# Kernel optimization log

Hardware: AMD Instinct MI355X
Metric: run time of the kernel (lower is better)

The kernel has to match this reference:

```python
import jax, jax.numpy as jnp
import numpy as np

B, S, D, H, DFF = 4, 2048, 512, 8, 2048
HD = D // H  # head dim = 64
LN_EPS = 1e-5


def setup_inputs() -> dict:
    key = jax.random.key(0)
    ks = jax.random.split(key, 12)
    sc = 0.02
    return {
        "x": jax.random.normal(ks[0], (B, S, D), jnp.float32),
        "Wq": jax.random.normal(ks[1], (D, D), jnp.float32) * sc,
        "bq": jnp.zeros((D,), jnp.float32),
        "Wk": jax.random.normal(ks[2], (D, D), jnp.float32) * sc,
        "bk": jnp.zeros((D,), jnp.float32),
        "Wv": jax.random.normal(ks[3], (D, D), jnp.float32) * sc,
        "bv": jnp.zeros((D,), jnp.float32),
        "W1": jax.random.normal(ks[4], (D, DFF), jnp.float32) * sc,
        "b1": jnp.zeros((DFF,), jnp.float32),
        "W2": jax.random.normal(ks[5], (DFF, D), jnp.float32) * sc,
        "b2": jnp.zeros((D,), jnp.float32),
        "gamma": jnp.ones((D,), jnp.float32),
        "beta": jnp.zeros((D,), jnp.float32),
    }


def reference(x, Wq, bq, Wk, bk, Wv, bv, W1, b1, W2, b2, gamma, beta):
    # Multi-head self-attention (explicit bmm -> softmax -> bmm chain)
    q = (x @ Wq + bq).reshape(B, S, H, HD)
    k = (x @ Wk + bk).reshape(B, S, H, HD)
    v = (x @ Wv + bv).reshape(B, S, H, HD)
    scores = jnp.einsum("bqhd,bkhd->bhqk", q, k) / jnp.sqrt(jnp.float32(HD))
    atn = jax.nn.softmax(scores, axis=-1)          # [B,H,S,S]
    attn_out = jnp.einsum("bhqk,bkhd->bqhd", atn, v).reshape(B, S, D)
    # FFN with residual + LayerNorm (residual around FFN only, as in source)
    h = jax.nn.relu(attn_out @ W1 + b1)
    y = h @ W2 + b2 + attn_out
    mu = jnp.mean(y, axis=-1, keepdims=True)
    var = jnp.var(y, axis=-1, keepdims=True)
    out = (y - mu) * jax.lax.rsqrt(var + LN_EPS) * gamma + beta
    return (out, atn)
```

## Files before the change

kernel.cpp:

```cpp
#include <hip/hip_runtime.h>
#include <hip/hip_bf16.h>

#define TPB 256
typedef long long ll;


using short8  = __attribute__((ext_vector_type(8))) short;
using floatx4 = __attribute__((ext_vector_type(4))) float;

__device__ __forceinline__ unsigned short f2bu(float f) {
    union { float f; unsigned int u; } v; v.f = f;
    unsigned int u = v.u;
    return (unsigned short)((u + 0x7fffu + ((u >> 16) & 1u)) >> 16);
}

__device__ __forceinline__ float bu2f(unsigned short us) {
    union { unsigned int u; float f; } v; v.u = ((unsigned int)us) << 16;
    return v.f;
}

__device__ __forceinline__ unsigned int cvtpk(float lo, float hi) {
    unsigned int r;
    asm volatile("v_cvt_pk_bf16_f32 %0, %1, %2" : "=v"(r) : "v"(lo), "v"(hi));
    return r;
}

__device__ __forceinline__ void gload16(const unsigned short* g, unsigned short* l) {
    __builtin_amdgcn_global_load_lds(
        (const __attribute__((address_space(1))) void*)g,
        (__attribute__((address_space(3))) void*)l, 16, 0, 0);
}

template<int BM, int BN, int EPI>
__device__ __forceinline__ void gemm_body(
    const unsigned short* __restrict__ Ap, const unsigned short* __restrict__ BTp,
    const float* __restrict__ bias, void* __restrict__ Cp,
    const unsigned short* __restrict__ Rb,
    int K, ll lda, ll ldb, ll ldc, int bx, int by,
    unsigned short* Asm, unsigned short* Bsm)
{
    constexpr int BK = 64;
    const int tid  = threadIdx.x;
    const int lane = tid & 63;
    const int wave = tid >> 6;
    const int wm = wave >> 1, wn = wave & 1;
    constexpr int WM = BM / 2, WN = BN / 2, FM = WM / 16, FN = WN / 16;

    const ll brow = (ll)bx * BM;
    const ll bcol = (ll)by * BN;
    const int srow = lane >> 3, scol = (lane & 7) << 3;

    floatx4 acc[FM][FN] = {};

    for (int k0 = 0; k0 < K; k0 += BK) {
        #pragma unroll
        for (int ii = 0; ii < BM / 32; ++ii) {
            int i = wave + ii * 4;
            gload16(Ap + (brow + i * 8 + srow) * lda + k0 + scol, Asm + i * 512);
        }
        #pragma unroll
        for (int ii = 0; ii < BN / 32; ++ii) {
            int i = wave + ii * 4;
            gload16(BTp + (bcol + i * 8 + srow) * ldb + k0 + scol, Bsm + i * 512);
        }
        __syncthreads();

        #pragma unroll
        for (int kk = 0; kk < BK; kk += 32) {
            short8 af[FM], bfr[FN];
            const int kidx = kk + ((lane >> 4) << 3);
            const int ar = wm * WM + (lane & 15);
            const int bc = wn * WN + (lane & 15);
            #pragma unroll
            for (int m = 0; m < FM; m++)
                af[m] = *(const short8*)&Asm[(ar + m * 16) * BK + kidx];
            #pragma unroll
            for (int n = 0; n < FN; n++)
                bfr[n] = *(const short8*)&Bsm[(bc + n * 16) * BK + kidx];
            #pragma unroll
            for (int m = 0; m < FM; m++)
                #pragma unroll
                for (int n = 0; n < FN; n++)
                    acc[m][n] = __builtin_amdgcn_mfma_f32_16x16x32_bf16(af[m], bfr[n], acc[m][n], 0, 0, 0);
        }
        __syncthreads();
    }

    const ll crow0 = brow + wm * WM + ((lane >> 4) << 2);
    const ll ccol0 = bcol + wn * WN + (lane & 15);
    #pragma unroll
    for (int m = 0; m < FM; m++) {
        #pragma unroll
        for (int j = 0; j < 4; j++) {
            ll row = crow0 + m * 16 + j;
            #pragma unroll
            for (int np = 0; np < FN; np += 2) {
                ll col0 = ccol0 + np * 16;
                ll col1 = col0 + 16;
                float v0 = acc[m][np][j]     + bias[col0];
                float v1 = acc[m][np + 1][j] + bias[col1];
                if constexpr (EPI == 3) {
                    v0 = v0 > 0.f ? v0 : 0.f;
                    v1 = v1 > 0.f ? v1 : 0.f;
                } else if constexpr (EPI == 6) {
                    v0 += bu2f(Rb[row * ldc + col0]);
                    v1 += bu2f(Rb[row * ldc + col1]);
                }
                unsigned int r = cvtpk(v0, v1);
                ((unsigned short*)Cp)[row * ldc + col0] = (unsigned short)r;
                ((unsigned short*)Cp)[row * ldc + col1] = (unsigned short)(r >> 16);
            }
        }
    }
}

template<int BM, int BN, int EPI>
__global__ __launch_bounds__(TPB) void gemm_k(
    const unsigned short* __restrict__ Ap, const unsigned short* __restrict__ BTp,
    const float* __restrict__ bias, void* __restrict__ Cp,
    const unsigned short* __restrict__ Rb,
    int K, ll lda, ll ldb, ll ldc)
{
    __shared__ unsigned short sh[BM * 64 + BN * 64];
    int nwg = gridDim.x * gridDim.y;
    int sid = blockIdx.y * gridDim.x + blockIdx.x;
    int cpx = nwg >> 3;
    int w = (sid & 7) * cpx + (sid >> 3);
    int bx = w % gridDim.x, by = w / gridDim.x;
    gemm_body<BM, BN, EPI>(Ap, BTp, bias, Cp, Rb, K, lda, ldb, ldc, bx, by,
                           sh, sh + BM * 64);
}

__device__ __forceinline__ void atnwrite_body(
    const unsigned short* __restrict__ qkv, const float* __restrict__ ilbuf,
    float* __restrict__ atn, int BH0, int n, unsigned short* sh)
{
    unsigned short* Qsm = sh;
    unsigned short* Ksm = sh + 8192;
    float* Pst = (float*)sh;

    const int tid = threadIdx.x, lane = tid & 63, wave = tid >> 6;
    const int c0 = lane & 15, g = lane >> 4;
    const int bh = BH0 + (n & 7) * 2 + ((n >> 3) & 1);
    const int qt = n >> 4;
    const int b = bh >> 3, h = bh & 7;

    const ll qbase  = ((ll)(b * 2048 + qt * 128)) * 1536 + h * 64;
    const ll kbase0 = ((ll)(b * 2048)) * 1536 + 512 + h * 64;
    const int srow = lane >> 3, scol = (lane & 7) << 3;

    #pragma unroll
    for (int ii = 0; ii < 4; ++ii) {
        int i = wave + ii * 4;
        gload16(qkv + qbase + (ll)(i * 8 + srow) * 1536 + scol, Qsm + i * 512);
    }
    __syncthreads();
    short8 qf[2][2];
    #pragma unroll
    for (int nq = 0; nq < 2; nq++)
        #pragma unroll
        for (int kk = 0; kk < 2; kk++)
            qf[nq][kk] = *(const short8*)&Qsm[(wave * 32 + nq * 16 + c0) * 64 + kk * 32 + g * 8];

    float il2[2];
    #pragma unroll
    for (int nq = 0; nq < 2; nq++)
        il2[nq] = ilbuf[(ll)bh * 2048 + qt * 128 + wave * 32 + nq * 16 + c0];

    float* myP = Pst + wave * 1024;

    for (int kb = 0; kb < 16; ++kb) {
        const ll koff = kbase0 + (ll)kb * 128 * 1536;
        #pragma unroll
        for (int ii = 0; ii < 4; ++ii) {
            int i = wave + ii * 4;
            gload16(qkv + koff + (ll)(i * 8 + srow) * 1536 + scol, Ksm + i * 512);
        }
        __syncthreads();

        floatx4 sacc[8][2] = {};
        #pragma unroll
        for (int kk = 0; kk < 2; kk++)
            #pragma unroll
            for (int mk = 0; mk < 8; mk++) {
                short8 kf = *(const short8*)&Ksm[(mk * 16 + c0) * 64 + kk * 32 + g * 8];
                #pragma unroll
                for (int nq = 0; nq < 2; nq++)
                    sacc[mk][nq] = __builtin_amdgcn_mfma_f32_16x16x32_bf16(kf, qf[nq][kk], sacc[mk][nq], 0, 0, 0);
            }

        #pragma unroll
        for (int mk = 0; mk < 8; mk++)
            #pragma unroll
            for (int nq = 0; nq < 2; nq++)
                #pragma unroll
                for (int r = 0; r < 4; r++)
                    sacc[mk][nq][r] = __expf(sacc[mk][nq][r] * 0.125f) * il2[nq];

        #pragma unroll
        for (int nq = 0; nq < 2; nq++) {
            #pragma unroll
            for (int hf = 0; hf < 2; hf++) {
                if ((c0 >> 3) == hf) {
                    int rho = c0 & 7;
                    #pragma unroll
                    for (int mk = 0; mk < 8; mk++) {
                        int k4 = mk * 4 + g;
                        ((floatx4*)myP)[rho * 32 + (k4 ^ rho)] = sacc[mk][nq];
                    }
                }
                const ll grow = (ll)bh * 2048 + qt * 128 + wave * 32 + nq * 16 + hf * 8;
                #pragma unroll
                for (int t = 0; t < 4; t++) {
                    int rr = t * 2 + (lane >> 5);
                    int k4r = lane & 31;
                    floatx4 v = ((const floatx4*)myP)[rr * 32 + (k4r ^ rr)];
                    __builtin_nontemporal_store(
                        v, (floatx4*)(atn + (grow + rr) * 2048 + kb * 128 + k4r * 4));
                }
            }
        }
        __syncthreads();
    }
}

__global__ __launch_bounds__(TPB) void attn1_k(
    const unsigned short* __restrict__ qkv, const unsigned short* __restrict__ vt,
    unsigned short* __restrict__ attnb, float* __restrict__ ilbuf)
{
    __shared__ unsigned short sh[32768];

    const int tid = threadIdx.x, lane = tid & 63, wave = tid >> 6;
    const int c0 = lane & 15, g = lane >> 4;
    const int srow = lane >> 3, scol = (lane & 7) << 3;

    const int raw = blockIdx.x + blockIdx.y * 16;
    const int n   = raw >> 3;
    const int bh  = (raw & 7) * 4 + (n >> 4);
    const int qt  = n & 15;
    const int b = bh >> 3, h = bh & 7;

    const ll qbase  = ((ll)(b * 2048 + qt * 128)) * 1536 + h * 64;
    const ll kbase0 = ((ll)(b * 2048)) * 1536 + 512 + h * 64;
    const unsigned short* vbase = vt + (ll)bh * 64 * 2048;

    #pragma unroll
    for (int ii = 0; ii < 4; ++ii) {
        int i = wave + ii * 4;
        gload16(qkv + qbase + (ll)(i * 8 + srow) * 1536 + scol, sh + i * 512);
    }
    __syncthreads();
    short8 qf[2][2];
    #pragma unroll
    for (int nq = 0; nq < 2; nq++)
        #pragma unroll
        for (int kk = 0; kk < 2; kk++)
            qf[nq][kk] = *(const short8*)&sh[(wave * 32 + nq * 16 + c0) * 64 + kk * 32 + g * 8];
    __syncthreads();

    floatx4 oaccT[4][2] = {};
    float l_run[2] = {0.f, 0.f};

    const int srcA = c0 + ((g & 1) << 5);
    const int srcB = srcA + 16;
    const bool hiG = (g >= 2);

#define STAGE_KV(kbx, bb) do {                                                   \
    const ll koff_ = kbase0 + (ll)(kbx) * 128 * 1536;                            \
    unsigned short* Kd_ = sh + ((bb) << 13);                                     \
    unsigned short* Vd_ = sh + 16384 + ((bb) << 13);                             \
    _Pragma("unroll")                                                            \
    for (int ii = 0; ii < 4; ++ii) { int i = wave + ii * 4;                      \
        gload16(qkv + koff_ + (ll)(i * 8 + srow) * 1536 + scol, Kd_ + i * 512); }\
    _Pragma("unroll")                                                            \
    for (int ii = 0; ii < 4; ++ii) { int i = wave + ii * 4; int s = i * 8 + srow;\
        gload16(vbase + (ll)(s >> 1) * 2048 + (kbx) * 128 + (s & 1) * 64 + scol, \
                Vd_ + i * 512); }                                                \
} while (0)

    STAGE_KV(0, 0);
    for (int kb = 0; kb < 16; ++kb) {
        const int cur = kb & 1;
        if (kb < 15) {
            STAGE_KV(kb + 1, cur ^ 1);
            asm volatile("s_waitcnt vmcnt(8)" ::: "memory");
        } else {
            asm volatile("s_waitcnt vmcnt(0)" ::: "memory");
        }
        __builtin_amdgcn_sched_barrier(0);
        __builtin_amdgcn_s_barrier();
        __builtin_amdgcn_sched_barrier(0);

        unsigned short* Kc = sh + (cur << 13);
        unsigned short* Vc = sh + 16384 + (cur << 13);

        floatx4 sacc[8][2] = {};
        #pragma unroll
        for (int kk = 0; kk < 2; kk++)
            #pragma unroll
            for (int mk = 0; mk < 8; mk++) {
                short8 kf = *(const short8*)&Kc[(mk * 16 + c0) * 64 + kk * 32 + g * 8];
                #pragma unroll
                for (int nq = 0; nq < 2; nq++)
                    sacc[mk][nq] = __builtin_amdgcn_mfma_f32_16x16x32_bf16(kf, qf[nq][kk], sacc[mk][nq], 0, 0, 0);
            }

        #pragma unroll
        for (int nq = 0; nq < 2; nq++) {
            float rs = 0.f;
            #pragma unroll
            for (int mk = 0; mk < 8; mk++)
                #pragma unroll
                for (int r = 0; r < 4; r++) {
                    float p = __expf(sacc[mk][nq][r] * 0.125f);
                    sacc[mk][nq][r] = p;
                    rs += p;
                }
            rs += __shfl_xor(rs, 16);
            rs += __shfl_xor(rs, 32);
            l_run[nq] += rs;
        }

        unsigned int P2[8][2][2];
        #pragma unroll
        for (int mk = 0; mk < 8; mk++)
            #pragma unroll
            for (int nq = 0; nq < 2; nq++) {
                P2[mk][nq][0] = cvtpk(sacc[mk][nq][0], sacc[mk][nq][1]);
                P2[mk][nq][1] = cvtpk(sacc[mk][nq][2], sacc[mk][nq][3]);
            }

        #pragma unroll
        for (int kk2 = 0; kk2 < 4; kk2++) {
            short8 pb[2];
            #pragma unroll
            for (int nq = 0; nq < 2; nq++) {
                unsigned int aLo0 = (unsigned int)__shfl((int)P2[2 * kk2][nq][0], srcA);
                unsigned int aHi0 = (unsigned int)__shfl((int)P2[2 * kk2 + 1][nq][0], srcA);
                unsigned int aLo1 = (unsigned int)__shfl((int)P2[2 * kk2][nq][1], srcA);
                unsigned int aHi1 = (unsigned int)__shfl((int)P2[2 * kk2 + 1][nq][1], srcA);
                unsigned int bLo0 = (unsigned int)__shfl((int)P2[2 * kk2][nq][0], srcB);
                unsigned int bHi0 = (unsigned int)__shfl((int)P2[2 * kk2 + 1][nq][0], srcB);
                unsigned int bLo1 = (unsigned int)__shfl((int)P2[2 * kk2][nq][1], srcB);
                unsigned int bHi1 = (unsigned int)__shfl((int)P2[2 * kk2 + 1][nq][1], srcB);
                union { unsigned int u[4]; short8 s; } pu;
                pu.u[0] = hiG ? aHi0 : aLo0;
                pu.u[1] = hiG ? aHi1 : aLo1;
                pu.u[2] = hiG ? bHi0 : bLo0;
                pu.u[3] = hiG ? bHi1 : bLo1;
                pb[nq] = pu.s;
            }
            #pragma unroll
            for (int mk2 = 0; mk2 < 4; mk2++) {
                short8 vf = *(const short8*)&Vc[(mk2 * 16 + c0) * 128 + kk2 * 32 + g * 8];
                #pragma unroll
                for (int nq = 0; nq < 2; nq++)
                    oaccT[mk2][nq] = __builtin_amdgcn_mfma_f32_16x16x32_bf16(vf, pb[nq], oaccT[mk2][nq], 0, 0, 0);
            }
        }
        __builtin_amdgcn_sched_barrier(0);
        __builtin_amdgcn_s_barrier();
        __builtin_amdgcn_sched_barrier(0);
    }
#undef STAGE_KV

    const float il[2] = { 1.0f / l_run[0], 1.0f / l_run[1] };

    #pragma unroll
    for (int nq = 0; nq < 2; nq++) {
        int qrow = qt * 128 + wave * 32 + nq * 16 + c0;
        ll row = (ll)b * 2048 + qrow;
        #pragma unroll
        for (int mk2 = 0; mk2 < 4; mk2++) {
            int col = h * 64 + mk2 * 16 + g * 4;
            unsigned int r0 = cvtpk(oaccT[mk2][nq][0] * il[nq], oaccT[mk2][nq][1] * il[nq]);
            unsigned int r1 = cvtpk(oaccT[mk2][nq][2] * il[nq], oaccT[mk2][nq][3] * il[nq]);
            int2 tb = { (int)r0, (int)r1 };
            *(int2*)&attnb[row * 512 + col] = tb;
        }
        if (g == 0) ilbuf[(ll)bh * 2048 + qrow] = il[nq];
    }
}

template<int BH0, int GX, int GY, int BM, int BN, int EPI>
__global__ __launch_bounds__(TPB) void fused_k(
    const unsigned short* __restrict__ qkv, const float* __restrict__ ilbuf,
    float* __restrict__ atn,
    const unsigned short* __restrict__ Ap, const unsigned short* __restrict__ BTp,
    const float* __restrict__ bias, void* __restrict__ Cp,
    const unsigned short* __restrict__ Rb,
    int K, ll lda, ll ldb, ll ldc)
{
    __shared__ unsigned short sh[16384];
    const int bid = blockIdx.x;
    if (bid < 256) {
        atnwrite_body(qkv, ilbuf, atn, BH0, bid, sh);
    } else {
        int sid = bid - 256;
        constexpr int NWG = GX * GY;
        int w = (sid & 7) * (NWG >> 3) + (sid >> 3);
        int bx = w % GX, by = w / GX;
        gemm_body<BM, BN, EPI>(Ap, BTp, bias, Cp, Rb, K, lda, ldb, ldc, bx, by,
                               sh, sh + BM * 64);
    }
}

__global__ __launch_bounds__(TPB) void ln_k(const unsigned short* __restrict__ y,
                                            const float* __restrict__ gamma,
                                            const float* __restrict__ beta,
                                            float* __restrict__ out)
{
    const int lane = threadIdx.x & 63;
    const ll row = (ll)blockIdx.x * 4 + (threadIdx.x >> 6);
    short8 v = *(const short8*)(y + row * 512 + lane * 8);
    float f[8];
    float s = 0.f, q = 0.f;
    #pragma unroll
    for (int j = 0; j < 8; j++) {
        f[j] = bu2f((unsigned short)v[j]);
        s += f[j]; q += f[j] * f[j];
    }
    #pragma unroll
    for (int off = 32; off; off >>= 1) { s += __shfl_xor(s, off); q += __shfl_xor(q, off); }
    const float mu  = s * (1.0f / 512.0f);
    const float var = q * (1.0f / 512.0f) - mu * mu;
    const float rs  = rsqrtf(var + 1e-5f);

    float4 g0 = *(const float4*)(gamma + lane * 8);
    float4 g1 = *(const float4*)(gamma + lane * 8 + 4);
    float4 e0 = *(const float4*)(beta  + lane * 8);
    float4 e1 = *(const float4*)(beta  + lane * 8 + 4);
    floatx4 o0, o1;
    o0[0] = (f[0] - mu) * rs * g0.x + e0.x;  o0[1] = (f[1] - mu) * rs * g0.y + e0.y;
    o0[2] = (f[2] - mu) * rs * g0.z + e0.z;  o0[3] = (f[3] - mu) * rs * g0.w + e0.w;
    o1[0] = (f[4] - mu) * rs * g1.x + e1.x;  o1[1] = (f[5] - mu) * rs * g1.y + e1.y;
    o1[2] = (f[6] - mu) * rs * g1.z + e1.z;  o1[3] = (f[7] - mu) * rs * g1.w + e1.w;
    __builtin_nontemporal_store(o0, (floatx4*)(out + row * 512 + lane * 8));
    __builtin_nontemporal_store(o1, (floatx4*)(out + row * 512 + lane * 8 + 4));
}

__global__ __launch_bounds__(TPB) void prep_k(
    const float* __restrict__ Wq, const float* __restrict__ Wk,
    const float* __restrict__ Wv, const float* __restrict__ W1,
    const float* __restrict__ W2,
    const float* __restrict__ bq, const float* __restrict__ bk,
    const float* __restrict__ bv,
    unsigned short* __restrict__ wtqkv, unsigned short* __restrict__ wt1,
    unsigned short* __restrict__ wt2, float* __restrict__ bqkv)
{
    __shared__ float t[32 * 33];
    const int bid = blockIdx.x;
    const float* W; unsigned short* WT; int K, N, tile;
    if (bid < 256)       { W = Wq; WT = wtqkv;             K = 512;  N = 512;  tile = bid; }
    else if (bid < 512)  { W = Wk; WT = wtqkv + 512 * 512; K = 512;  N = 512;  tile = bid - 256; }
    else if (bid < 768)  { W = Wv; WT = wtqkv + 1024 * 512;K = 512;  N = 512;  tile = bid - 512; }
    else if (bid < 1792) { W = W1; WT = wt1;               K = 512;  N = 2048; tile = bid - 768; }
    else if (bid < 2816) { W = W2; WT = wt2;               K = 2048; N = 512;  tile = bid - 1792; }
    else {
        int i = (bid - 2816) * TPB + threadIdx.x;
        if (i < 512)       bqkv[i] = bq[i];
        else if (i < 1024) bqkv[i] = bk[i - 512];
        else if (i < 1536) bqkv[i] = bv[i - 1024];
        return;
    }
    const int nx = N >> 5;
    const int n0 = (tile % nx) * 32, k0 = (tile / nx) * 32;
    const int tx = threadIdx.x & 31, ty = threadIdx.x >> 5;
    #pragma unroll
    for (int i = ty; i < 32; i += 8) t[i * 33 + tx] = W[(ll)(k0 + i) * N + n0 + tx];
    __syncthreads();
    #pragma unroll
    for (int i = ty; i < 32; i += 8) WT[(ll)(n0 + i) * K + k0 + tx] = f2bu(t[tx * 33 + i]);
}

__global__ __launch_bounds__(TPB) void castx_k(const float* __restrict__ x,
                                               unsigned short* __restrict__ o, ll n)
{
    ll i = ((ll)blockIdx.x * TPB + threadIdx.x) * 4;
    if (i >= n) return;
    float4 v = *(const float4*)(x + i);
    unsigned int r0 = cvtpk(v.x, v.y), r1 = cvtpk(v.z, v.w);
    int2 t = { (int)r0, (int)r1 };
    *(int2*)(o + i) = t;
}

__global__ __launch_bounds__(TPB) void transv_k(const unsigned short* __restrict__ qkv,
                                                unsigned short* __restrict__ vt)
{
    const int z = blockIdx.y;  const int b = z >> 3, h = z & 7;
    const int s0 = blockIdx.x * 64;
    __shared__ unsigned short t[64][72];
    const unsigned short* src = qkv + ((ll)(b * 2048 + s0)) * 1536 + 1024 + h * 64;
    for (int c = threadIdx.x; c < 512; c += TPB) {
        int r = c >> 3, c8 = (c & 7) << 3;
        *(int4*)&t[r][c8] = *(const int4*)(src + (ll)r * 1536 + c8);
    }
    __syncthreads();
    unsigned short* dst = vt + (ll)z * 64 * 2048 + s0;
    for (int c = threadIdx.x; c < 512; c += TPB) {
        int hd = c >> 3, s8 = (c & 7) << 3;
        unsigned short tmp[8];
        #pragma unroll
        for (int j = 0; j < 8; j++) tmp[j] = t[s8 + j][hd];
        *(int4*)(dst + (ll)hd * 2048 + s8) = *(const int4*)tmp;
    }
}

extern "C" void kernel_launch(void* const* d_in, const int* in_sizes, int n_in,
                              void* d_out, int out_size, void* d_ws, size_t ws_size,
                              hipStream_t stream)
{
    (void)in_sizes; (void)n_in; (void)out_size; (void)ws_size;
    const float* x     = (const float*)d_in[0];
    const float* Wq    = (const float*)d_in[1];
    const float* bq    = (const float*)d_in[2];
    const float* Wk    = (const float*)d_in[3];
    const float* bk    = (const float*)d_in[4];
    const float* Wv    = (const float*)d_in[5];
    const float* bv    = (const float*)d_in[6];
    const float* W1    = (const float*)d_in[7];
    const float* b1    = (const float*)d_in[8];
    const float* W2    = (const float*)d_in[9];
    const float* b2    = (const float*)d_in[10];
    const float* gamma = (const float*)d_in[11];
    const float* beta  = (const float*)d_in[12];

    char* ws = (char*)d_ws;
    size_t off = 0;
    auto alloc = [&](size_t bytes) -> char* {
        char* p = ws + off; off += (bytes + 255) & ~(size_t)255; return p;
    };
    unsigned short* xb    = (unsigned short*)alloc(8192ll * 512 * 2);
    unsigned short* wtqkv = (unsigned short*)alloc(1536ll * 512 * 2);
    unsigned short* wt1   = (unsigned short*)alloc(2048ll * 512 * 2);
    unsigned short* wt2   = (unsigned short*)alloc(512ll * 2048 * 2);
    float*          bqkv  = (float*)alloc(1536 * 4);
    unsigned short* qkv   = (unsigned short*)alloc(8192ll * 1536 * 2);
    unsigned short* vt    = (unsigned short*)alloc(32ll * 64 * 2048 * 2);
    unsigned short* attnb = (unsigned short*)alloc(8192ll * 512 * 2);
    unsigned short* hmid  = (unsigned short*)alloc(8192ll * 2048 * 2);
    unsigned short* ybuf  = (unsigned short*)alloc(8192ll * 512 * 2);
    float*          ilbuf = (float*)alloc(32ll * 2048 * 4);

    float* outp = (float*)d_out;
    float* atn  = outp + 4194304;

    castx_k<<<4096, TPB, 0, stream>>>(x, xb, 8192ll * 512);
    prep_k<<<2822, TPB, 0, stream>>>(Wq, Wk, Wv, W1, W2, bq, bk, bv,
                                     wtqkv, wt1, wt2, bqkv);

    gemm_k<128, 128, 0><<<dim3(64, 12, 1), TPB, 0, stream>>>(
        xb, wtqkv, bqkv, qkv, nullptr, 512, 512, 512, 1536);

    transv_k<<<dim3(32, 32), TPB, 0, stream>>>(qkv, vt);

    attn1_k<<<dim3(16, 32), TPB, 0, stream>>>(qkv, vt, attnb, ilbuf);

    fused_k<0, 64, 16, 128, 128, 3><<<256 + 1024, TPB, 0, stream>>>(
        qkv, ilbuf, atn,
        attnb, wt1, b1, hmid, nullptr, 512, 512, 512, 2048);

    fused_k<16, 128, 4, 64, 128, 6><<<256 + 512, TPB, 0, stream>>>(
        qkv, ilbuf, atn,
        hmid, wt2, b2, ybuf, attnb, 2048, 2048, 2048, 512);

    ln_k<<<2048, TPB, 0, stream>>>(ybuf, gamma, beta, outp);
}
```

Measured before the change: 315.7 us.

## Swizzle LDS tiles, fold softmax scale into QKV GEMM, drop P shuffles

Applies an XOR swizzle to the LDS tile layouts for GEMM, Q, K and V loads so fragment reads avoid bank conflicts. It folds the 1/sqrt(d) scale into the QKV GEMM epilogue for the Q columns and removes the multiply before exp. In attention, the PV product now uses 16x16x16 MFMA so the P accumulator layout can feed it directly, which removes the cross-lane shuffle repacking. The x cast kernel is merged into prep_k to save a launch. Pre-scaling Q in bf16 adds slightly different rounding, and the smaller MFMA issues more instructions.

```diff
diff --git a/kernel.cpp b/kernel.cpp
--- a/kernel.cpp
+++ b/kernel.cpp
@@ -6,6 +6,7 @@
 
 
 using short8  = __attribute__((ext_vector_type(8))) short;
+using short4v = __attribute__((ext_vector_type(4))) short;
 using floatx4 = __attribute__((ext_vector_type(4))) float;
 
 __device__ __forceinline__ unsigned short f2bu(float f) {
@@ -23,6 +24,17 @@
     unsigned int r;
     asm volatile("v_cvt_pk_bf16_f32 %0, %1, %2" : "=v"(r) : "v"(lo), "v"(hi));
     return r;
+}
+
+__device__ __forceinline__ floatx4 mfma16(short4v a, short4v b, floatx4 c) {
+#if __has_builtin(__builtin_amdgcn_mfma_f32_16x16x16bf16_1k)
+    return __builtin_amdgcn_mfma_f32_16x16x16bf16_1k(a, b, c, 0, 0, 0);
+#else
+    floatx4 d;
+    asm volatile("v_mfma_f32_16x16x16_bf16 %0, %1, %2, %3"
+                 : "=v"(d) : "v"(a), "v"(b), "v"(c));
+    return d;
+#endif
 }
 
 __device__ __forceinline__ void gload16(const unsigned short* g, unsigned short* l) {
@@ -48,7 +60,9 @@
 
     const ll brow = (ll)bx * BM;
     const ll bcol = (ll)by * BN;
-    const int srow = lane >> 3, scol = (lane & 7) << 3;
+    const int srow = lane >> 3;
+    const int ssw  = (((lane & 7) ^ srow)) << 3;
+    const int kswz = (lane & 7) << 3;
 
     floatx4 acc[FM][FN] = {};
 
@@ -56,19 +70,19 @@
         #pragma unroll
         for (int ii = 0; ii < BM / 32; ++ii) {
             int i = wave + ii * 4;
-            gload16(Ap + (brow + i * 8 + srow) * lda + k0 + scol, Asm + i * 512);
+            gload16(Ap + (brow + i * 8 + srow) * lda + k0 + ssw, Asm + i * 512);
         }
         #pragma unroll
         for (int ii = 0; ii < BN / 32; ++ii) {
             int i = wave + ii * 4;
-            gload16(BTp + (bcol + i * 8 + srow) * ldb + k0 + scol, Bsm + i * 512);
+            gload16(BTp + (bcol + i * 8 + srow) * ldb + k0 + ssw, Bsm + i * 512);
         }
         __syncthreads();
 
         #pragma unroll
         for (int kk = 0; kk < BK; kk += 32) {
             short8 af[FM], bfr[FN];
-            const int kidx = kk + ((lane >> 4) << 3);
+            const int kidx = (kk + ((lane >> 4) << 3)) ^ kswz;
             const int ar = wm * WM + (lane & 15);
             const int bc = wn * WN + (lane & 15);
             #pragma unroll
@@ -105,6 +119,9 @@
                 } else if constexpr (EPI == 6) {
                     v0 += bu2f(Rb[row * ldc + col0]);
                     v1 += bu2f(Rb[row * ldc + col1]);
+                } else if constexpr (EPI == 7) {
+                    if (col0 < 512) v0 *= 0.125f;
+                    if (col1 < 512) v1 *= 0.125f;
                 }
                 unsigned int r = cvtpk(v0, v1);
                 ((unsigned short*)Cp)[row * ldc + col0] = (unsigned short)r;
@@ -147,12 +164,14 @@
 
     const ll qbase  = ((ll)(b * 2048 + qt * 128)) * 1536 + h * 64;
     const ll kbase0 = ((ll)(b * 2048)) * 1536 + 512 + h * 64;
-    const int srow = lane >> 3, scol = (lane & 7) << 3;
+    const int srow = lane >> 3;
+    const int ssw  = (((lane & 7) ^ srow)) << 3;
+    const int kswz = (lane & 7) << 3;
 
     #pragma unroll
     for (int ii = 0; ii < 4; ++ii) {
         int i = wave + ii * 4;
-        gload16(qkv + qbase + (ll)(i * 8 + srow) * 1536 + scol, Qsm + i * 512);
+        gload16(qkv + qbase + (ll)(i * 8 + srow) * 1536 + ssw, Qsm + i * 512);
     }
     __syncthreads();
     short8 qf[2][2];
@@ -160,7 +179,7 @@
     for (int nq = 0; nq < 2; nq++)
         #pragma unroll
         for (int kk = 0; kk < 2; kk++)
-            qf[nq][kk] = *(const short8*)&Qsm[(wave * 32 + nq * 16 + c0) * 64 + kk * 32 + g * 8];
+            qf[nq][kk] = *(const short8*)&Qsm[(wave * 32 + nq * 16 + c0) * 64 + ((kk * 32 + g * 8) ^ kswz)];
 
     float il2[2];
     #pragma unroll
@@ -174,7 +193,7 @@
         #pragma unroll
         for (int ii = 0; ii < 4; ++ii) {
             int i = wave + ii * 4;
-            gload16(qkv + koff + (ll)(i * 8 + srow) * 1536 + scol, Ksm + i * 512);
+            gload16(qkv + koff + (ll)(i * 8 + srow) * 1536 + ssw, Ksm + i * 512);
         }
         __syncthreads();
 
@@ -183,7 +202,7 @@
         for (int kk = 0; kk < 2; kk++)
             #pragma unroll
             for (int mk = 0; mk < 8; mk++) {
-                short8 kf = *(const short8*)&Ksm[(mk * 16 + c0) * 64 + kk * 32 + g * 8];
+                short8 kf = *(const short8*)&Ksm[(mk * 16 + c0) * 64 + ((kk * 32 + g * 8) ^ kswz)];
                 #pragma unroll
                 for (int nq = 0; nq < 2; nq++)
                     sacc[mk][nq] = __builtin_amdgcn_mfma_f32_16x16x32_bf16(kf, qf[nq][kk], sacc[mk][nq], 0, 0, 0);
@@ -195,7 +214,7 @@
             for (int nq = 0; nq < 2; nq++)
                 #pragma unroll
                 for (int r = 0; r < 4; r++)
-                    sacc[mk][nq][r] = __expf(sacc[mk][nq][r] * 0.125f) * il2[nq];
+                    sacc[mk][nq][r] = __expf(sacc[mk][nq][r]) * il2[nq];
 
         #pragma unroll
         for (int nq = 0; nq < 2; nq++) {
@@ -232,7 +251,9 @@
 
     const int tid = threadIdx.x, lane = tid & 63, wave = tid >> 6;
     const int c0 = lane & 15, g = lane >> 4;
-    const int srow = lane >> 3, scol = (lane & 7) << 3;
+    const int srow = lane >> 3;
+    const int ssw  = (((lane & 7) ^ srow)) << 3;
+    const int kswz = (lane & 7) << 3;
 
     const int raw = blockIdx.x + blockIdx.y * 16;
     const int n   = raw >> 3;
@@ -247,7 +268,7 @@
     #pragma unroll
     for (int ii = 0; ii < 4; ++ii) {
         int i = wave + ii * 4;
-        gload16(qkv + qbase + (ll)(i * 8 + srow) * 1536 + scol, sh + i * 512);
+        gload16(qkv + qbase + (ll)(i * 8 + srow) * 1536 + ssw, sh + i * 512);
     }
     __syncthreads();
     short8 qf[2][2];
@@ -255,15 +276,11 @@
     for (int nq = 0; nq < 2; nq++)
         #pragma unroll
         for (int kk = 0; kk < 2; kk++)
-            qf[nq][kk] = *(const short8*)&sh[(wave * 32 + nq * 16 + c0) * 64 + kk * 32 + g * 8];
+            qf[nq][kk] = *(const short8*)&sh[(wave * 32 + nq * 16 + c0) * 64 + ((kk * 32 + g * 8) ^ kswz)];
     __syncthreads();
 
     floatx4 oaccT[4][2] = {};
     float l_run[2] = {0.f, 0.f};
-
-    const int srcA = c0 + ((g & 1) << 5);
-    const int srcB = srcA + 16;
-    const bool hiG = (g >= 2);
 
 #define STAGE_KV(kbx, bb) do {                                                   \
     const ll koff_ = kbase0 + (ll)(kbx) * 128 * 1536;                            \
@@ -271,10 +288,11 @@
     unsigned short* Vd_ = sh + 16384 + ((bb) << 13);                             \
     _Pragma("unroll")                                                            \
     for (int ii = 0; ii < 4; ++ii) { int i = wave + ii * 4;                      \
-        gload16(qkv + koff_ + (ll)(i * 8 + srow) * 1536 + scol, Kd_ + i * 512); }\
+        gload16(qkv + koff_ + (ll)(i * 8 + srow) * 1536 + ssw, Kd_ + i * 512); } \
     _Pragma("unroll")                                                            \
     for (int ii = 0; ii < 4; ++ii) { int i = wave + ii * 4; int s = i * 8 + srow;\
-        gload16(vbase + (ll)(s >> 1) * 2048 + (kbx) * 128 + (s & 1) * 64 + scol, \
+        int vrow = s >> 1; int vslot = ((s & 1) << 3) | (lane & 7);              \
+        gload16(vbase + (ll)vrow * 2048 + (kbx) * 128 + ((vslot ^ (vrow & 7)) << 3), \
                 Vd_ + i * 512); }                                                \
 } while (0)
 
@@ -299,7 +317,7 @@
         for (int kk = 0; kk < 2; kk++)
             #pragma unroll
             for (int mk = 0; mk < 8; mk++) {
-                short8 kf = *(const short8*)&Kc[(mk * 16 + c0) * 64 + kk * 32 + g * 8];
+                short8 kf = *(const short8*)&Kc[(mk * 16 + c0) * 64 + ((kk * 32 + g * 8) ^ kswz)];
                 #pragma unroll
                 for (int nq = 0; nq < 2; nq++)
                     sacc[mk][nq] = __builtin_amdgcn_mfma_f32_16x16x32_bf16(kf, qf[nq][kk], sacc[mk][nq], 0, 0, 0);
@@ -312,7 +330,7 @@
             for (int mk = 0; mk < 8; mk++)
                 #pragma unroll
                 for (int r = 0; r < 4; r++) {
-                    float p = __expf(sacc[mk][nq][r] * 0.125f);
+                    float p = __expf(sacc[mk][nq][r]);
                     sacc[mk][nq][r] = p;
                     rs += p;
                 }
@@ -321,41 +339,22 @@
             l_run[nq] += rs;
         }
 
-        unsigned int P2[8][2][2];
-        #pragma unroll
-        for (int mk = 0; mk < 8; mk++)
+        #pragma unroll
+        for (int mk = 0; mk < 8; mk++) {
+            short4v pb[2];
             #pragma unroll
             for (int nq = 0; nq < 2; nq++) {
-                P2[mk][nq][0] = cvtpk(sacc[mk][nq][0], sacc[mk][nq][1]);
-                P2[mk][nq][1] = cvtpk(sacc[mk][nq][2], sacc[mk][nq][3]);
-            }
-
-        #pragma unroll
-        for (int kk2 = 0; kk2 < 4; kk2++) {
-            short8 pb[2];
-            #pragma unroll
-            for (int nq = 0; nq < 2; nq++) {
-                unsigned int aLo0 = (unsigned int)__shfl((int)P2[2 * kk2][nq][0], srcA);
-                unsigned int aHi0 = (unsigned int)__shfl((int)P2[2 * kk2 + 1][nq][0], srcA);
-                unsigned int aLo1 = (unsigned int)__shfl((int)P2[2 * kk2][nq][1], srcA);
-                unsigned int aHi1 = (unsigned int)__shfl((int)P2[2 * kk2 + 1][nq][1], srcA);
-                unsigned int bLo0 = (unsigned int)__shfl((int)P2[2 * kk2][nq][0], srcB);
-                unsigned int bHi0 = (unsigned int)__shfl((int)P2[2 * kk2 + 1][nq][0], srcB);
-                unsigned int bLo1 = (unsigned int)__shfl((int)P2[2 * kk2][nq][1], srcB);
-                unsigned int bHi1 = (unsigned int)__shfl((int)P2[2 * kk2 + 1][nq][1], srcB);
-                union { unsigned int u[4]; short8 s; } pu;
-                pu.u[0] = hiG ? aHi0 : aLo0;
-                pu.u[1] = hiG ? aHi1 : aLo1;
-                pu.u[2] = hiG ? bHi0 : bLo0;
-                pu.u[3] = hiG ? bHi1 : bLo1;
+                union { unsigned int u[2]; short4v s; } pu;
+                pu.u[0] = cvtpk(sacc[mk][nq][0], sacc[mk][nq][1]);
+                pu.u[1] = cvtpk(sacc[mk][nq][2], sacc[mk][nq][3]);
                 pb[nq] = pu.s;
             }
             #pragma unroll
             for (int mk2 = 0; mk2 < 4; mk2++) {
-                short8 vf = *(const short8*)&Vc[(mk2 * 16 + c0) * 128 + kk2 * 32 + g * 8];
+                short4v vf = *(const short4v*)&Vc[(mk2 * 16 + c0) * 128 + ((mk * 16 + g * 4) ^ kswz)];
                 #pragma unroll
                 for (int nq = 0; nq < 2; nq++)
-                    oaccT[mk2][nq] = __builtin_amdgcn_mfma_f32_16x16x32_bf16(vf, pb[nq], oaccT[mk2][nq], 0, 0, 0);
+                    oaccT[mk2][nq] = mfma16(vf, pb[nq], oaccT[mk2][nq]);
             }
         }
         __builtin_amdgcn_sched_barrier(0);
@@ -444,9 +443,10 @@
     const float* __restrict__ Wv, const float* __restrict__ W1,
     const float* __restrict__ W2,
     const float* __restrict__ bq, const float* __restrict__ bk,
-    const float* __restrict__ bv,
+    const float* __restrict__ bv, const float* __restrict__ x,
     unsigned short* __restrict__ wtqkv, unsigned short* __restrict__ wt1,
-    unsigned short* __restrict__ wt2, float* __restrict__ bqkv)
+    unsigned short* __restrict__ wt2, float* __restrict__ bqkv,
+    unsigned short* __restrict__ xb)
 {
     __shared__ float t[32 * 33];
     const int bid = blockIdx.x;
@@ -456,12 +456,19 @@
     else if (bid < 768)  { W = Wv; WT = wtqkv + 1024 * 512;K = 512;  N = 512;  tile = bid - 512; }
     else if (bid < 1792) { W = W1; WT = wt1;               K = 512;  N = 2048; tile = bid - 768; }
     else if (bid < 2816) { W = W2; WT = wt2;               K = 2048; N = 512;  tile = bid - 1792; }
-    else {
+    else if (bid < 2822) {
         int i = (bid - 2816) * TPB + threadIdx.x;
         if (i < 512)       bqkv[i] = bq[i];
         else if (i < 1024) bqkv[i] = bk[i - 512];
         else if (i < 1536) bqkv[i] = bv[i - 1024];
         return;
+    } else {
+        ll i = ((ll)(bid - 2822) * TPB + threadIdx.x) * 4;
+        float4 v = *(const float4*)(x + i);
+        unsigned int r0 = cvtpk(v.x, v.y), r1 = cvtpk(v.z, v.w);
+        int2 tt = { (int)r0, (int)r1 };
+        *(int2*)(xb + i) = tt;
+        return;
     }
     const int nx = N >> 5;
     const int n0 = (tile % nx) * 32, k0 = (tile / nx) * 32;
@@ -471,17 +478,6 @@
     __syncthreads();
     #pragma unroll
     for (int i = ty; i < 32; i += 8) WT[(ll)(n0 + i) * K + k0 + tx] = f2bu(t[tx * 33 + i]);
-}
-
-__global__ __launch_bounds__(TPB) void castx_k(const float* __restrict__ x,
-                                               unsigned short* __restrict__ o, ll n)
-{
-    ll i = ((ll)blockIdx.x * TPB + threadIdx.x) * 4;
-    if (i >= n) return;
-    float4 v = *(const float4*)(x + i);
-    unsigned int r0 = cvtpk(v.x, v.y), r1 = cvtpk(v.z, v.w);
-    int2 t = { (int)r0, (int)r1 };
-    *(int2*)(o + i) = t;
 }
 
 __global__ __launch_bounds__(TPB) void transv_k(const unsigned short* __restrict__ qkv,
@@ -545,11 +541,10 @@
     float* outp = (float*)d_out;
     float* atn  = outp + 4194304;
 
-    castx_k<<<4096, TPB, 0, stream>>>(x, xb, 8192ll * 512);
-    prep_k<<<2822, TPB, 0, stream>>>(Wq, Wk, Wv, W1, W2, bq, bk, bv,
-                                     wtqkv, wt1, wt2, bqkv);
-
-    gemm_k<128, 128, 0><<<dim3(64, 12, 1), TPB, 0, stream>>>(
+    prep_k<<<2822 + 4096, TPB, 0, stream>>>(Wq, Wk, Wv, W1, W2, bq, bk, bv, x,
+                                            wtqkv, wt1, wt2, bqkv, xb);
+
+    gemm_k<128, 128, 7><<<dim3(64, 12, 1), TPB, 0, stream>>>(
         xb, wtqkv, bqkv, qkv, nullptr, 512, 512, 512, 1536);
 
     transv_k<<<dim3(32, 32), TPB, 0, stream>>>(qkv, vt);
```

New measurement: 275.1 us. 1.15x faster.
